# Kernel tuning notes

Hardware: AMD Instinct MI355X
Metric: run time of the kernel (lower is better)

Reference implementation:

```python
import jax, jax.numpy as jnp
import numpy as np

N_NODES = 100000
N_NEIGH = 10
DIM = 256
N_LAYERS = 3


def setup_inputs() -> dict:
    key = jax.random.key(0)
    ks = jax.random.split(key, 8)
    x = jax.random.normal(ks[0], (N_NODES, DIM), dtype=jnp.float32)
    adj = jax.random.randint(ks[1], (N_NODES, N_NEIGH), 0, N_NODES, dtype=jnp.int32)
    # per-layer SAGE weights: Linear(2*D -> D), stored as [2D, D] for x @ W
    scale = 0.05
    W0 = jax.random.normal(ks[2], (2 * DIM, DIM), dtype=jnp.float32) * scale
    W1 = jax.random.normal(ks[3], (2 * DIM, DIM), dtype=jnp.float32) * scale
    W2 = jax.random.normal(ks[4], (2 * DIM, DIM), dtype=jnp.float32) * scale
    b0 = jnp.zeros((DIM,), dtype=jnp.float32)
    b1 = jnp.zeros((DIM,), dtype=jnp.float32)
    b2 = jnp.zeros((DIM,), dtype=jnp.float32)
    return {"x": x, "adj": adj, "W0": W0, "b0": b0, "W1": W1, "b1": b1,
            "W2": W2, "b2": b2}


def reference(x, adj, W0, b0, W1, b1, W2, b2):
    """GraphSAGE: per layer, gather sampled neighbors [N,K,D], mean over K,
    concat with self embedding, linear [2D->D], ReLU on all but last layer."""
    layers = [(W0, b0), (W1, b1), (W2, b2)]
    h = x
    for i, (W, b) in enumerate(layers):
        neigh = jnp.mean(h[adj], axis=1)                 # [N, K, D] -> [N, D]
        h = jnp.concatenate([h, neigh], axis=1) @ W + b  # [N, 2D] @ [2D, D]
        if i < len(layers) - 1:
            h = jax.nn.relu(h)
    return h
```

## Files before the change

### kernel.cpp

```cpp
#include <hip/hip_runtime.h>
#include <stdint.h>

#define NN 100000
#define NK 10
#define D  256
#define D2 512
#define MT 32

typedef short bf16x8 __attribute__((ext_vector_type(8)));
typedef float f32x4  __attribute__((ext_vector_type(4)));

__device__ __forceinline__ uint16_t f2bf(float f) {
  uint32_t u = __float_as_uint(f);
  u += 0x7fffu + ((u >> 16) & 1u);
  return (uint16_t)(u >> 16);
}
__device__ __forceinline__ uint32_t pack2(float a, float b) {
  return (uint32_t)f2bf(a) | ((uint32_t)f2bf(b) << 16);
}

__global__ void pack_w(const float* __restrict__ W, uint16_t* __restrict__ Wp) {
  int idx   = blockIdx.x * blockDim.x + threadIdx.x;
  int lane  = idx & 63;
  int ntile = (idx >> 6) & 15;
  int kstep = idx >> 10;
  int n  = ntile * 16 + (lane & 15);
  int k0 = kstep * 32 + (lane >> 4) * 8;
  float v[8];
#pragma unroll
  for (int j = 0; j < 8; j++) v[j] = W[(size_t)(k0 + j) * D + n];
  uint4 o;
  o.x = pack2(v[0], v[1]);
  o.y = pack2(v[2], v[3]);
  o.z = pack2(v[4], v[5]);
  o.w = pack2(v[6], v[7]);
  ((uint4*)Wp)[idx] = o;
}

template <bool IN_BF16, bool OUT_BF16>
__global__ __launch_bounds__(256, 5) void sage_layer(
    const void* __restrict__ hin_v,
    const int*  __restrict__ adj,
    const uint16_t* __restrict__ Wp,
    const float* __restrict__ bias,
    void*       __restrict__ hout_v,
    const int relu)
{
  __shared__ uint4 lds4[MT * 64];
  const int t  = threadIdx.x;
  const int m0 = blockIdx.x * MT;

#pragma unroll
  for (int i = 0; i < 4; i++) {
    int cidx = t + i * 256;
    int r = cidx >> 5;
    int c = cidx & 31;
    uint4 o;
    int node = m0 + r;
    if (IN_BF16) {
      o = *(const uint4*)((const uint16_t*)hin_v + (size_t)node * D + c * 8);
    } else {
      const float4* p = (const float4*)((const float*)hin_v + (size_t)node * D + c * 8);
      float4 v0 = p[0], v1 = p[1];
      o.x = pack2(v0.x, v0.y); o.y = pack2(v0.z, v0.w);
      o.z = pack2(v1.x, v1.y); o.w = pack2(v1.z, v1.w);
    }
    lds4[r * 64 + (c ^ (r & 15))] = o;
  }

  {
    const int half = t >> 5;
    const int l32  = t & 31;
#pragma unroll 1
    for (int i = 0; i < 4; i++) {
      int r = i * 8 + half;
      int node = m0 + r;
      float a0=0.f,a1=0.f,a2=0.f,a3=0.f,a4=0.f,a5=0.f,a6=0.f,a7=0.f;
#pragma unroll
      for (int k = 0; k < NK; k++) {
        int nb = adj[node * NK + k];
        if (IN_BF16) {
          uint4 v = *(const uint4*)((const uint16_t*)hin_v + (size_t)nb * D + l32 * 8);
          a0 += __uint_as_float(v.x << 16);
          a1 += __uint_as_float(v.x & 0xffff0000u);
          a2 += __uint_as_float(v.y << 16);
          a3 += __uint_as_float(v.y & 0xffff0000u);
          a4 += __uint_as_float(v.z << 16);
          a5 += __uint_as_float(v.z & 0xffff0000u);
          a6 += __uint_as_float(v.w << 16);
          a7 += __uint_as_float(v.w & 0xffff0000u);
        } else {
          const float4* p = (const float4*)((const float*)hin_v + (size_t)nb * D + l32 * 8);
          float4 v0 = p[0], v1 = p[1];
          a0 += v0.x; a1 += v0.y; a2 += v0.z; a3 += v0.w;
          a4 += v1.x; a5 += v1.y; a6 += v1.z; a7 += v1.w;
        }
      }
      const float s = 1.0f / (float)NK;
      uint4 o;
      o.x = pack2(a0 * s, a1 * s);
      o.y = pack2(a2 * s, a3 * s);
      o.z = pack2(a4 * s, a5 * s);
      o.w = pack2(a6 * s, a7 * s);
      int c = 32 + l32;
      lds4[r * 64 + (c ^ (r & 15))] = o;
    }
  }

  __syncthreads();

  const int w    = t >> 6;
  const int l    = t & 63;
  const int quad = l >> 4;
  const int l16  = l & 15;

  f32x4 acc[2][4];
#pragma unroll
  for (int mt = 0; mt < 2; mt++)
#pragma unroll
    for (int nt = 0; nt < 4; nt++)
      acc[mt][nt] = (f32x4){0.f, 0.f, 0.f, 0.f};

  const uint4* wp4 = (const uint4*)Wp;

#pragma unroll 2
  for (int ks = 0; ks < 16; ks++) {
    bf16x8 af[2], bfr[4];
#pragma unroll
    for (int mt = 0; mt < 2; mt++) {
      int row = mt * 16 + l16;
      int c   = ks * 4 + quad;
      af[mt] = *((const bf16x8*)&lds4[row * 64 + (c ^ (row & 15))]);
    }
#pragma unroll
    for (int nt = 0; nt < 4; nt++) {
      bfr[nt] = *((const bf16x8*)&wp4[(ks * 16 + (w * 4 + nt)) * 64 + l]);
    }
#pragma unroll
    for (int mt = 0; mt < 2; mt++)
#pragma unroll
      for (int nt = 0; nt < 4; nt++)
        acc[mt][nt] = __builtin_amdgcn_mfma_f32_16x16x32_bf16(
            af[mt], bfr[nt], acc[mt][nt], 0, 0, 0);
  }

#pragma unroll
  for (int mt = 0; mt < 2; mt++) {
#pragma unroll
    for (int i = 0; i < 4; i++) {
      int rr = m0 + mt * 16 + quad * 4 + i;
#pragma unroll
      for (int nt = 0; nt < 4; nt++) {
        int col = w * 64 + nt * 16 + l16;
        float v = acc[mt][nt][i] + bias[col];
        if (relu) v = fmaxf(v, 0.0f);
        if (OUT_BF16)
          ((uint16_t*)hout_v)[(size_t)rr * D + col] = f2bf(v);
        else
          ((float*)hout_v)[(size_t)rr * D + col] = v;
      }
    }
  }
}

extern "C" void kernel_launch(void* const* d_in, const int* in_sizes, int n_in,
                              void* d_out, int out_size, void* d_ws, size_t ws_size,
                              hipStream_t stream) {
  const float* x   = (const float*)d_in[0];
  const int*   adj = (const int*)d_in[1];
  const float* W0  = (const float*)d_in[2];
  const float* b0  = (const float*)d_in[3];
  const float* W1  = (const float*)d_in[4];
  const float* b1  = (const float*)d_in[5];
  const float* W2  = (const float*)d_in[6];
  const float* b2  = (const float*)d_in[7];
  float* out = (float*)d_out;

  uint16_t* ws  = (uint16_t*)d_ws;
  uint16_t* Wp0 = ws;
  uint16_t* Wp1 = Wp0 + D2 * D;
  uint16_t* Wp2 = Wp1 + D2 * D;
  uint16_t* hB  = Wp2 + D2 * D;
  uint16_t* hA  = (uint16_t*)d_out;

  pack_w<<<64, 256, 0, stream>>>(W0, Wp0);
  pack_w<<<64, 256, 0, stream>>>(W1, Wp1);
  pack_w<<<64, 256, 0, stream>>>(W2, Wp2);

  const int grid = NN / MT;
  sage_layer<false, true ><<<grid, 256, 0, stream>>>(x,  adj, Wp0, b0, hA,  1);
  sage_layer<true,  true ><<<grid, 256, 0, stream>>>(hA, adj, Wp1, b1, hB,  1);
  sage_layer<true,  false><<<grid, 256, 0, stream>>>(hB, adj, Wp2, b2, out, 0);
}
```

Before: 516.1 us.

## Gather neighbors from int8 per-row quantized embedding tables

Adds a pre-pass that quantizes x to int8 with a per-row absmax scale. Each layer now also writes an int8 copy plus per-row scale of its ReLU output, computing the row max with shuffles and an LDS reduction. The neighbor mean-gather then reads 8 bytes per lane plus one scale instead of 16–32 bytes, cutting the random-gather traffic that dominates the kernel. The cost is an extra quantization pass over x, extra byte writes and a block sync in the epilogue, and lower precision in the neighbor aggregate that could affect tolerance.

```diff
diff --git a/kernel.cpp b/kernel.cpp
--- a/kernel.cpp
+++ b/kernel.cpp
@@ -17,6 +17,24 @@
 }
 __device__ __forceinline__ uint32_t pack2(float a, float b) {
   return (uint32_t)f2bf(a) | ((uint32_t)f2bf(b) << 16);
+}
+
+__global__ __launch_bounds__(256) void quant_x(const float* __restrict__ x,
+                                               uint8_t* __restrict__ q8,
+                                               float*   __restrict__ qs) {
+  int node = blockIdx.x * 4 + (threadIdx.x >> 6);
+  int lane = threadIdx.x & 63;
+  const float4 v = *(const float4*)(x + (size_t)node * D + lane * 4);
+  float m = fmaxf(fmaxf(fabsf(v.x), fabsf(v.y)), fmaxf(fabsf(v.z), fabsf(v.w)));
+#pragma unroll
+  for (int d = 1; d < 64; d <<= 1) m = fmaxf(m, __shfl_xor(m, d, 64));
+  float inv = m > 1e-30f ? 127.0f / m : 0.0f;
+  int q0 = (int)rintf(v.x * inv), q1 = (int)rintf(v.y * inv);
+  int q2 = (int)rintf(v.z * inv), q3 = (int)rintf(v.w * inv);
+  uint32_t p = (uint32_t)(q0 & 0xff) | ((uint32_t)(q1 & 0xff) << 8) |
+               ((uint32_t)(q2 & 0xff) << 16) | ((uint32_t)(q3 & 0xff) << 24);
+  ((uint32_t*)(q8 + (size_t)node * D))[lane] = p;
+  if (lane == 0) qs[node] = m * (1.0f / 127.0f);
 }
 
 __global__ void pack_w(const float* __restrict__ W, uint16_t* __restrict__ Wp) {
@@ -37,14 +55,17 @@
   ((uint4*)Wp)[idx] = o;
 }
 
-template <bool IN_BF16, bool OUT_BF16>
+template <bool SELF_F32, bool QOUT>
 __global__ __launch_bounds__(256, 5) void sage_layer(
-    const void* __restrict__ hin_v,
-    const int*  __restrict__ adj,
+    const void*     __restrict__ hin_v,
+    const uint8_t*  __restrict__ qtab,
+    const float*    __restrict__ qsc,
+    const int*      __restrict__ adj,
     const uint16_t* __restrict__ Wp,
-    const float* __restrict__ bias,
-    void*       __restrict__ hout_v,
-    const int relu)
+    const float*    __restrict__ bias,
+    void*           __restrict__ hout_v,
+    uint8_t*        __restrict__ q8out,
+    float*          __restrict__ qsout)
 {
   __shared__ uint4 lds4[MT * 64];
   const int t  = threadIdx.x;
@@ -55,15 +76,15 @@
     int cidx = t + i * 256;
     int r = cidx >> 5;
     int c = cidx & 31;
+    int node = m0 + r;
     uint4 o;
-    int node = m0 + r;
-    if (IN_BF16) {
-      o = *(const uint4*)((const uint16_t*)hin_v + (size_t)node * D + c * 8);
-    } else {
+    if (SELF_F32) {
       const float4* p = (const float4*)((const float*)hin_v + (size_t)node * D + c * 8);
       float4 v0 = p[0], v1 = p[1];
       o.x = pack2(v0.x, v0.y); o.y = pack2(v0.z, v0.w);
       o.z = pack2(v1.x, v1.y); o.w = pack2(v1.z, v1.w);
+    } else {
+      o = *(const uint4*)((const uint16_t*)hin_v + (size_t)node * D + c * 8);
     }
     lds4[r * 64 + (c ^ (r & 15))] = o;
   }
@@ -79,29 +100,23 @@
 #pragma unroll
       for (int k = 0; k < NK; k++) {
         int nb = adj[node * NK + k];
-        if (IN_BF16) {
-          uint4 v = *(const uint4*)((const uint16_t*)hin_v + (size_t)nb * D + l32 * 8);
-          a0 += __uint_as_float(v.x << 16);
-          a1 += __uint_as_float(v.x & 0xffff0000u);
-          a2 += __uint_as_float(v.y << 16);
-          a3 += __uint_as_float(v.y & 0xffff0000u);
-          a4 += __uint_as_float(v.z << 16);
-          a5 += __uint_as_float(v.z & 0xffff0000u);
-          a6 += __uint_as_float(v.w << 16);
-          a7 += __uint_as_float(v.w & 0xffff0000u);
-        } else {
-          const float4* p = (const float4*)((const float*)hin_v + (size_t)nb * D + l32 * 8);
-          float4 v0 = p[0], v1 = p[1];
-          a0 += v0.x; a1 += v0.y; a2 += v0.z; a3 += v0.w;
-          a4 += v1.x; a5 += v1.y; a6 += v1.z; a7 += v1.w;
-        }
-      }
-      const float s = 1.0f / (float)NK;
+        float s = qsc[nb];
+        uint2 v = *(const uint2*)(qtab + (size_t)nb * D + l32 * 8);
+        a0 += s * (float)(int8_t)(v.x);
+        a1 += s * (float)(int8_t)(v.x >> 8);
+        a2 += s * (float)(int8_t)(v.x >> 16);
+        a3 += s * (float)(int8_t)(v.x >> 24);
+        a4 += s * (float)(int8_t)(v.y);
+        a5 += s * (float)(int8_t)(v.y >> 8);
+        a6 += s * (float)(int8_t)(v.y >> 16);
+        a7 += s * (float)(int8_t)(v.y >> 24);
+      }
+      const float sc = 1.0f / (float)NK;
       uint4 o;
-      o.x = pack2(a0 * s, a1 * s);
-      o.y = pack2(a2 * s, a3 * s);
-      o.z = pack2(a4 * s, a5 * s);
-      o.w = pack2(a6 * s, a7 * s);
+      o.x = pack2(a0 * sc, a1 * sc);
+      o.y = pack2(a2 * sc, a3 * sc);
+      o.z = pack2(a4 * sc, a5 * sc);
+      o.w = pack2(a6 * sc, a7 * sc);
       int c = 32 + l32;
       lds4[r * 64 + (c ^ (r & 15))] = o;
     }
@@ -144,23 +159,74 @@
             af[mt], bfr[nt], acc[mt][nt], 0, 0, 0);
   }
 
-#pragma unroll
-  for (int mt = 0; mt < 2; mt++) {
+  float lmax[2][4];
+#pragma unroll
+  for (int mt = 0; mt < 2; mt++)
+#pragma unroll
+    for (int i = 0; i < 4; i++) lmax[mt][i] = 0.0f;
+
+#pragma unroll
+  for (int mt = 0; mt < 2; mt++)
+#pragma unroll
+    for (int nt = 0; nt < 4; nt++)
+#pragma unroll
+      for (int i = 0; i < 4; i++) {
+        int col = w * 64 + nt * 16 + l16;
+        float v = acc[mt][nt][i] + bias[col];
+        if (QOUT) v = fmaxf(v, 0.0f);
+        acc[mt][nt][i] = v;
+        if (QOUT) lmax[mt][i] = fmaxf(lmax[mt][i], v);
+      }
+
+  float inv[2][4];
+  if (QOUT) {
+#pragma unroll
+    for (int d = 1; d < 16; d <<= 1)
+#pragma unroll
+      for (int mt = 0; mt < 2; mt++)
+#pragma unroll
+        for (int i = 0; i < 4; i++)
+          lmax[mt][i] = fmaxf(lmax[mt][i], __shfl_xor(lmax[mt][i], d, 64));
+    __syncthreads();
+    float* rmax = (float*)lds4;
+    if (l16 == 0) {
+#pragma unroll
+      for (int mt = 0; mt < 2; mt++)
+#pragma unroll
+        for (int i = 0; i < 4; i++)
+          rmax[(mt * 16 + quad * 4 + i) * 4 + w] = lmax[mt][i];
+    }
+    __syncthreads();
+#pragma unroll
+    for (int mt = 0; mt < 2; mt++)
+#pragma unroll
+      for (int i = 0; i < 4; i++) {
+        int row = mt * 16 + quad * 4 + i;
+        float m = fmaxf(fmaxf(rmax[row * 4 + 0], rmax[row * 4 + 1]),
+                        fmaxf(rmax[row * 4 + 2], rmax[row * 4 + 3]));
+        inv[mt][i] = m > 1e-30f ? 127.0f / m : 0.0f;
+        if (w == 0 && l16 == 0) qsout[m0 + row] = m * (1.0f / 127.0f);
+      }
+  }
+
+#pragma unroll
+  for (int mt = 0; mt < 2; mt++)
 #pragma unroll
     for (int i = 0; i < 4; i++) {
       int rr = m0 + mt * 16 + quad * 4 + i;
 #pragma unroll
       for (int nt = 0; nt < 4; nt++) {
         int col = w * 64 + nt * 16 + l16;
-        float v = acc[mt][nt][i] + bias[col];
-        if (relu) v = fmaxf(v, 0.0f);
-        if (OUT_BF16)
+        float v = acc[mt][nt][i];
+        if (QOUT) {
           ((uint16_t*)hout_v)[(size_t)rr * D + col] = f2bf(v);
-        else
+          int q = (int)rintf(v * inv[mt][i]);
+          q8out[(size_t)rr * D + col] = (uint8_t)(q & 0xff);
+        } else {
           ((float*)hout_v)[(size_t)rr * D + col] = v;
-      }
-    }
-  }
+        }
+      }
+    }
 }
 
 extern "C" void kernel_launch(void* const* d_in, const int* in_sizes, int n_in,
@@ -176,19 +242,28 @@
   const float* b2  = (const float*)d_in[7];
   float* out = (float*)d_out;
 
+  uint8_t*  dob = (uint8_t*)d_out;
+  uint16_t* hA  = (uint16_t*)dob;
+  uint8_t*  hA8 = dob + 51200000;
+  uint8_t*  x8  = dob + 76800000;
+
   uint16_t* ws  = (uint16_t*)d_ws;
   uint16_t* Wp0 = ws;
   uint16_t* Wp1 = Wp0 + D2 * D;
   uint16_t* Wp2 = Wp1 + D2 * D;
   uint16_t* hB  = Wp2 + D2 * D;
-  uint16_t* hA  = (uint16_t*)d_out;
-
+  uint8_t*  hB8 = (uint8_t*)(hB + (size_t)NN * D);
+  float*    xs  = (float*)(hB8 + (size_t)NN * D);
+  float*    hAs = xs + NN;
+  float*    hBs = hAs + NN;
+
+  quant_x<<<NN / 4, 256, 0, stream>>>(x, x8, xs);
   pack_w<<<64, 256, 0, stream>>>(W0, Wp0);
   pack_w<<<64, 256, 0, stream>>>(W1, Wp1);
   pack_w<<<64, 256, 0, stream>>>(W2, Wp2);
 
   const int grid = NN / MT;
-  sage_layer<false, true ><<<grid, 256, 0, stream>>>(x,  adj, Wp0, b0, hA,  1);
-  sage_layer<true,  true ><<<grid, 256, 0, stream>>>(hA, adj, Wp1, b1, hB,  1);
-  sage_layer<true,  false><<<grid, 256, 0, stream>>>(hB, adj, Wp2, b2, out, 0);
-}
+  sage_layer<true,  true ><<<grid, 256, 0, stream>>>(x,  x8,  xs,  adj, Wp0, b0, hA,  hA8, hAs);
+  sage_layer<false, true ><<<grid, 256, 0, stream>>>(hA, hA8, hAs, adj, Wp1, b1, hB,  hB8, hBs);
+  sage_layer<false, false><<<grid, 256, 0, stream>>>(hB, hB8, hBs, adj, Wp2, b2, out, nullptr, nullptr);
+}
```

Result: faster. 457.1 us (-11.4%).
